# Kernel optimization log

Measured on AMD Instinct MI355X. Metric: run time of the kernel, lower is better.

## Reference

```python
import jax, jax.numpy as jnp
import numpy as np

LEAKY_ALPHA = 0.2  # LeakyReLU negative slope from init arg `alpha`


def setup_inputs() -> dict:
    key = jax.random.key(0)
    k1, k2, k3, k4 = jax.random.split(key, 4)
    B, N, Fin, Fout = 8, 2048, 256, 256
    h = jax.random.normal(k1, (B, N, Fin), dtype=jnp.float32)
    adj = jax.random.randint(k2, (N, N), 0, 2, dtype=jnp.int32)
    W = jax.random.normal(k3, (Fin, Fout), dtype=jnp.float32) * (1.414 * (6.0 / (Fin + Fout)) ** 0.5)
    a = jax.random.normal(k4, (2 * Fout, 1), dtype=jnp.float32) * (1.414 * (6.0 / (2 * Fout + 1)) ** 0.5)
    return {"h": h, "adj": adj, "W": W, "a": a}


def reference(h, adj, W, a):
    # h: (B, N, Fin), adj: (N, N) int {0,1}, W: (Fin, Fout), a: (2*Fout, 1)
    Fout = W.shape[1]
    Wh = jnp.einsum('bnf,fo->bno', h, W)            # (B, N, Fout)
    a1 = a[:Fout, 0]                                  # attends to target node i
    a2 = a[Fout:, 0]                                  # attends to source node j
    # a^T [Wh_i || Wh_j] == (Wh_i . a1) + (Wh_j . a2); LeakyReLU applied after, as in original
    s_i = Wh @ a1                                     # (B, N)
    s_j = Wh @ a2                                     # (B, N)
    e = jax.nn.leaky_relu(s_i[:, :, None] + s_j[:, None, :], negative_slope=LEAKY_ALPHA)  # (B, N, N)
    N = Wh.shape[1]
    mask = (adj > 0) | jnp.eye(N, dtype=bool)         # adjacency + self-loops
    e = jnp.where(mask[None, :, :], e, -jnp.inf)
    attention = jax.nn.softmax(e, axis=-1)            # dropout is identity in eval
    attention = jnp.nan_to_num(attention, nan=0.0)
    h_prime = jnp.einsum('bij,bjo->bio', attention, Wh)  # (B, N, Fout)
    return jax.nn.elu(h_prime)                        # concat=True -> ELU
```

## Files before the change

### kernel.cpp

```cpp
#include <hip/hip_runtime.h>

typedef unsigned short u16;
typedef unsigned int   u32;
typedef unsigned long long u64;

typedef __bf16 bf16x8 __attribute__((ext_vector_type(8)));
typedef float  f32x4  __attribute__((ext_vector_type(4)));

#define MFMA_BF16(a,b,c) __builtin_amdgcn_mfma_f32_16x16x32_bf16((a),(b),(c),0,0,0)

__device__ __forceinline__ float bf2f(u16 u) {
    return __uint_as_float(((u32)u) << 16);
}
__device__ __forceinline__ u16 f2bf(float x) {
    u32 u = __float_as_uint(x);
    u += 0x7fffu + ((u >> 16) & 1u);
    return (u16)(u >> 16);
}
__device__ __forceinline__ float ldany(const void* p, size_t i, int f32) {
    return f32 ? ((const float*)p)[i] : bf2f(((const u16*)p)[i]);
}
__device__ __forceinline__ int detect_f32(const u32* hw) {
    u32 w = hw[threadIdx.x & 63];
    int e = (w >> 23) & 0xFF;
    u64 m = __ballot(e >= 64 && e <= 190);
    return __popcll(m) >= 32 ? 1 : 0;
}

__global__ __launch_bounds__(256) void k0(const void* __restrict__ w, const void* __restrict__ a,
                                          u16* __restrict__ wt, float* __restrict__ wa1,
                                          float* __restrict__ wa2, const u32* __restrict__ hw) {
    int f32 = detect_f32(hw);
    int k = blockIdx.x, o = threadIdx.x;
    float wv = ldany(w, (size_t)k * 256 + o, f32);
    wt[o * 256 + k] = f2bf(wv);
    float p1 = wv * ldany(a, o, f32);
    float p2 = wv * ldany(a, 256 + o, f32);
    for (int d = 32; d; d >>= 1) { p1 += __shfl_down(p1, d); p2 += __shfl_down(p2, d); }
    __shared__ float s1[4], s2[4];
    int wid = o >> 6, lane = o & 63;
    if (lane == 0) { s1[wid] = p1; s2[wid] = p2; }
    __syncthreads();
    if (o == 0) { wa1[k] = s1[0] + s1[1] + s1[2] + s1[3]; wa2[k] = s2[0] + s2[1] + s2[2] + s2[3]; }
}

__global__ __launch_bounds__(256) void k1m(const int* __restrict__ adj, u64* __restrict__ mb64) {
    int t = threadIdx.x;
    int wv = t >> 6, lane = t & 63;
    #pragma unroll
    for (int q = 0; q < 4; q++) {
        int idx = blockIdx.x * 16 + wv * 4 + q;
        int mrow = idx >> 5, c = idx & 31;
        int j = c * 64 + lane;
        bool bit = (adj[(size_t)mrow * 2048 + j] > 0) || (j == mrow);
        u64 m = __ballot(bit);
        if (lane == 0) mb64[(size_t)mrow * 32 + c] = m;
    }
}

struct __align__(16) K2LDS {
    u16 At[64 * 68];
    union { u16 Bt[256 * 68]; u16 Ct[256 * 68]; };
    float wa1s[256], wa2s[256];
    float s1[64], s2[64];
};
__global__ __launch_bounds__(512) void k2(const void* __restrict__ h, const u16* __restrict__ wt,
                                          const float* __restrict__ wa1, const float* __restrict__ wa2,
                                          u16* __restrict__ whbt,
                                          float* __restrict__ sig, float* __restrict__ sjg) {
    __shared__ K2LDS L;
    int f32 = detect_f32((const u32*)h);
    int m0 = blockIdx.x * 64;
    int b  = m0 >> 11;
    int n0 = m0 & 2047;
    int t = threadIdx.x;
    int wid = t >> 6, lane = t & 63, ln = lane & 15, qd = lane >> 4;

    if (t < 256) { L.wa1s[t] = wa1[t]; L.wa2s[t] = wa2[t]; }
    if (t < 64) { L.s1[t] = 0.f; L.s2[t] = 0.f; }
    __syncthreads();

    float a1 = 0.f, a2 = 0.f;

    f32x4 acc[4][2];
    for (int mi = 0; mi < 4; mi++)
        for (int ni = 0; ni < 2; ni++)
            acc[mi][ni] = (f32x4){0.f, 0.f, 0.f, 0.f};

    for (int c = 0; c < 4; c++) {
        int k0c = c * 64;
        {
            int r = t >> 3, s = t & 7;
            float xv[8]; u16 uv[8];
            if (f32) {
                const float* src = (const float*)h + (size_t)(m0 + r) * 256 + k0c + s * 8;
                f32x4 x0 = *(const f32x4*)src;
                f32x4 x1 = *(const f32x4*)(src + 4);
                #pragma unroll
                for (int q = 0; q < 4; q++) { xv[q] = x0[q]; xv[4 + q] = x1[q]; }
                #pragma unroll
                for (int q = 0; q < 8; q++) uv[q] = f2bf(xv[q]);
            } else {
                const u16* src = (const u16*)h + (size_t)(m0 + r) * 256 + k0c + s * 8;
                *(uint4*)uv = *(const uint4*)src;
                #pragma unroll
                for (int q = 0; q < 8; q++) xv[q] = bf2f(uv[q]);
            }
            *(uint4*)&L.At[r * 68 + s * 8] = *(uint4*)uv;
            float pa = 0.f, pb = 0.f;
            #pragma unroll
            for (int q = 0; q < 8; q++) {
                pa += xv[q] * L.wa1s[k0c + s * 8 + q];
                pb += xv[q] * L.wa2s[k0c + s * 8 + q];
            }
            a1 += pa; a2 += pb;
        }
        #pragma unroll
        for (int p = 0; p < 4; p++) {
            int f = (t >> 3) + p * 64, s = t & 7;
            *(uint4*)&L.Bt[f * 68 + s * 8] =
                *(const uint4*)(wt + (size_t)f * 256 + k0c + s * 8);
        }
        __syncthreads();
        for (int ks = 0; ks < 2; ks++) {
            bf16x8 af[4], bfr[2];
            for (int mi = 0; mi < 4; mi++)
                af[mi] = *(const bf16x8*)&L.At[(mi * 16 + ln) * 68 + ks * 32 + qd * 8];
            for (int ni = 0; ni < 2; ni++)
                bfr[ni] = *(const bf16x8*)&L.Bt[(wid * 32 + ni * 16 + ln) * 68 + ks * 32 + qd * 8];
            for (int mi = 0; mi < 4; mi++)
                for (int ni = 0; ni < 2; ni++)
                    acc[mi][ni] = MFMA_BF16(af[mi], bfr[ni], acc[mi][ni]);
        }
        __syncthreads();
    }

    atomicAdd(&L.s1[t >> 3], a1);
    atomicAdd(&L.s2[t >> 3], a2);

    for (int mi = 0; mi < 4; mi++) {
        for (int ni = 0; ni < 2; ni++) {
            int f = wid * 32 + ni * 16 + ln;
            int n = mi * 16 + qd * 4;
            u16 v[4];
            for (int r = 0; r < 4; r++) v[r] = f2bf(acc[mi][ni][r]);
            *(uint2*)&L.Ct[f * 68 + n] = *(uint2*)v;
        }
    }
    __syncthreads();
    if (t < 64) { sig[m0 + t] = L.s1[t]; sjg[m0 + t] = L.s2[t]; }
    {
        int fr = t >> 1, hf = t & 1;
        size_t base = (size_t)b * 524288 + (size_t)fr * 2048 + n0;
        #pragma unroll
        for (int k = 0; k < 4; k++) {
            int s = hf * 4 + k;
            uint4 v = *(uint4*)&L.Ct[fr * 68 + s * 8];
            *(uint4*)(whbt + base + s * 8) = v;
        }
    }
}

__global__ __launch_bounds__(512) void k3n(const float* __restrict__ sig, const float* __restrict__ sjg,
                                           float* __restrict__ u1g, float* __restrict__ u2g,
                                           u32* __restrict__ vpackg, u16* __restrict__ sjbfg) {
    int b = blockIdx.x;
    int t = threadIdx.x;
    const float* sjb = sjg + (size_t)b * 2048;
    float mx = -3.4e38f;
    #pragma unroll
    for (int p = 0; p < 4; p++) mx = fmaxf(mx, sjb[t + p * 512]);
    for (int d = 32; d; d >>= 1) mx = fmaxf(mx, __shfl_xor(mx, d));
    __shared__ float wmax[8];
    int wid = t >> 6, lane = t & 63;
    if (lane == 0) wmax[wid] = mx;
    __syncthreads();
    float Mb = fmaxf(fmaxf(fmaxf(wmax[0], wmax[1]), fmaxf(wmax[2], wmax[3])),
                     fmaxf(fmaxf(wmax[4], wmax[5]), fmaxf(wmax[6], wmax[7])));
    #pragma unroll
    for (int p = 0; p < 4; p++) {
        int j = t + p * 512;
        float sjv = sjb[j];
        float vj  = __expf(sjv - Mb);
        float v2j = __expf(0.2f * (sjv - Mb));
        vpackg[b * 2048 + j] = (u32)f2bf(vj) | ((u32)f2bf(v2j) << 16);
        sjbfg[b * 2048 + j]  = f2bf(sjv);
        float siv = sig[b * 2048 + j];
        float x = siv + Mb;
        float K = fmaxf(x, 0.2f * x);
        u1g[b * 2048 + j] = __expf(x - K);
        u2g[b * 2048 + j] = __expf(0.2f * x - K);
    }
}

struct __align__(16) K4LDS {
    u32   vpack[2048];
    u16   sjb[2048];
    u64   mw[64 * 33];
    float u1[64], u2[64], nsi[64], inv[64];
    float lred[1024];
    u16   Pt[2][8192];
    int   claim[2];
};
__global__ __launch_bounds__(1024, 4) void k4(const float* __restrict__ sig,
                                              const float* __restrict__ u1g, const float* __restrict__ u2g,
                                              const u32* __restrict__ vpackg, const u16* __restrict__ sjbfg,
                                              const u64* __restrict__ mb64, const u16* __restrict__ whbt,
                                              void* __restrict__ out, const void* __restrict__ hdet,
                                              int* __restrict__ cnt) {
    __shared__ K4LDS L;
    int f32 = detect_f32((const u32*)hdet);
    int t = threadIdx.x;
    if (t == 0) {
        int xcd = __builtin_amdgcn_s_getreg(63508) & 7;
        int bsel = 0, tile = 0;
        #pragma unroll
        for (int k = 0; k < 8; k++) {
            int bb = (xcd + k) & 7;
            int tt = atomicAdd(&cnt[bb], 1);
            if (tt < 32) { bsel = bb; tile = tt; break; }
        }
        L.claim[0] = bsel; L.claim[1] = tile;
    }
    __syncthreads();
    int b  = L.claim[0];
    int i0 = L.claim[1] * 64;
    int wid = t >> 6, lane = t & 63, ln = lane & 15, qd = lane >> 4;
    const u16* wb = whbt + (size_t)b * 524288 + (size_t)wid * 16 * 2048;
    float lacc = 0.f;

    bf16x8 br[2][4];
    #define LOAD_B(cc, bb) do {                                             \
        int j0_ = (cc) * 128;                                               \
        _Pragma("unroll")                                                   \
        for (int ks = 0; ks < 4; ks++)                                      \
            br[bb][ks] = *(const bf16x8*)(wb +                              \
                (size_t)ln * 2048 + j0_ + ks * 32 + qd * 8);                \
    } while (0)

    #define PGEN(cc, bb) do {                                               \
        int r_ = t & 63, o_ = t >> 6;                                       \
        int jb_ = (cc) * 128 + o_ * 8;                                      \
        uint4 pkA_ = *(const uint4*)&L.vpack[jb_];                          \
        uint4 pkB_ = *(const uint4*)&L.vpack[jb_ + 4];                      \
        uint4 sj4_ = *(const uint4*)&L.sjb[jb_];                            \
        u32 mb_ = (u32)(L.mw[r_ * 33 + 2 * (cc) + (o_ >> 3)]                \
                        >> ((o_ & 7) * 8)) & 0xffu;                         \
        float u1_ = L.u1[r_], u2_ = L.u2[r_], nsi_ = L.nsi[r_];             \
        u32 pr_[4];                                                         \
        _Pragma("unroll")                                                   \
        for (int pk = 0; pk < 4; pk++) {                                    \
            u32 vw0_ = (pk == 0) ? pkA_.x : (pk == 1) ? pkA_.z              \
                     : (pk == 2) ? pkB_.x : pkB_.z;                         \
            u32 vw1_ = (pk == 0) ? pkA_.y : (pk == 1) ? pkA_.w              \
                     : (pk == 2) ? pkB_.y : pkB_.w;                         \
            u32 sw_ = (pk == 0) ? sj4_.x : (pk == 1) ? sj4_.y               \
                     : (pk == 2) ? sj4_.z : sj4_.w;                         \
            float sj0_ = __uint_as_float(sw_ << 16);                        \
            float sj1_ = __uint_as_float(sw_ & 0xffff0000u);                \
            float p0_, p1_;                                                 \
            {                                                               \
                bool pos = sj0_ > nsi_;                                     \
                float vv = __uint_as_float(pos ? (vw0_ << 16)               \
                                               : ((vw0_ >> 16) << 16));     \
                p0_ = (pos ? u1_ : u2_) * vv;                               \
                p0_ = ((mb_ >> (2 * pk)) & 1u) ? p0_ : 0.f;                 \
            }                                                               \
            {                                                               \
                bool pos = sj1_ > nsi_;                                     \
                float vv = __uint_as_float(pos ? (vw1_ << 16)               \
                                               : ((vw1_ >> 16) << 16));     \
                p1_ = (pos ? u1_ : u2_) * vv;                               \
                p1_ = ((mb_ >> (2 * pk + 1)) & 1u) ? p1_ : 0.f;             \
            }                                                               \
            lacc += p0_ + p1_;                                              \
            pr_[pk] = __builtin_amdgcn_perm(__float_as_uint(p1_),           \
                                            __float_as_uint(p0_),           \
                                            0x07060302u);                   \
        }                                                                   \
        *(uint4*)&L.Pt[bb][t * 8] = *(uint4*)pr_;                           \
    } while (0)

    LOAD_B(0, 0);
    for (int p = 0; p < 2; p++) { int idx = t + p * 1024; L.vpack[idx] = vpackg[b * 2048 + idx]; }
    ((u32*)L.sjb)[t] = ((const u32*)(sjbfg + (size_t)b * 2048))[t];
    for (int p = 0; p < 2; p++) {
        int idx = t + p * 1024;
        int r = idx >> 5, c = idx & 31;
        L.mw[r * 33 + c] = mb64[(size_t)(i0 + r) * 32 + c];
    }
    if (t < 64) {
        int row = b * 2048 + i0 + t;
        L.u1[t] = u1g[row]; L.u2[t] = u2g[row]; L.nsi[t] = -sig[row];
    }
    __syncthreads();
    PGEN(0, 0);

    f32x4 acc[4];
    for (int mi = 0; mi < 4; mi++)
        acc[mi] = (f32x4){0.f, 0.f, 0.f, 0.f};

    #define STEP(c, cur, nxt) do {                                          \
        __syncthreads();                                                    \
        if ((c) < 15) { LOAD_B((c) + 1, nxt); PGEN((c) + 1, nxt); }         \
        __builtin_amdgcn_s_setprio(1);                                      \
        _Pragma("unroll")                                                   \
        for (int ks = 0; ks < 4; ks++) {                                    \
            bf16x8 af[4];                                                   \
            _Pragma("unroll")                                               \
            for (int mi = 0; mi < 4; mi++)                                  \
                af[mi] = *(const bf16x8*)&L.Pt[cur][((ks * 4 + qd) * 64 +   \
                                                     mi * 16 + ln) * 8];    \
            _Pragma("unroll")                                               \
            for (int mi = 0; mi < 4; mi++)                                  \
                acc[mi] = MFMA_BF16(af[mi], br[cur][ks], acc[mi]);          \
        }                                                                   \
        __builtin_amdgcn_s_setprio(0);                                      \
    } while (0)

    for (int cc = 0; cc < 8; cc++) {
        STEP(2 * cc,     0, 1);
        STEP(2 * cc + 1, 1, 0);
    }

    __syncthreads();
    L.lred[t] = lacc;
    __syncthreads();
    if (t < 64) {
        float s = 0.f;
        #pragma unroll
        for (int q = 0; q < 16; q++) s += L.lred[q * 64 + t];
        L.inv[t] = 1.0f / s;
    }
    __syncthreads();

    {
        int fg = wid * 16 + ln;
        for (int mi = 0; mi < 4; mi++) {
            for (int reg = 0; reg < 4; reg++) {
                int rl = mi * 16 + qd * 4 + reg;
                float hp = acc[mi][reg] * L.inv[rl];
                float y = hp > 0.f ? hp : (__expf(hp) - 1.f);
                size_t idx = (size_t)(b * 2048 + i0 + rl) * 256 + fg;
                if (f32) ((float*)out)[idx] = y;
                else     ((u16*)out)[idx]   = f2bf(y);
            }
        }
    }
    #undef LOAD_B
    #undef PGEN
    #undef STEP
}

extern "C" void kernel_launch(void* const* d_in, const int* in_sizes, int n_in,
                              void* d_out, int out_size, void* d_ws, size_t ws_size,
                              hipStream_t stream) {
    const void* h   = d_in[0];
    const int*  adj = (const int*)d_in[1];
    const void* W   = d_in[2];
    const void* a   = d_in[3];

    char* ws = (char*)d_ws;
    u16*   WT    = (u16*)  (ws + 0);
    float* si    = (float*)(ws + 131072);
    float* sj    = (float*)(ws + 196608);
    float* u1    = (float*)(ws + 262144);
    float* u2    = (float*)(ws + 327680);
    u32*   vpack = (u32*)  (ws + 458752);
    u16*   sjbf  = (u16*)  (ws + 524288);
    u64*   mb64  = (u64*)  (ws + 557056);
    u16*   whbt  = (u16*)  (ws + 1081344);
    float* Wa1   = (float*)(ws + 9469952);
    float* Wa2   = (float*)(ws + 9470976);
    int*   cnt   = (int*)  (ws + 9472000);

    hipMemsetAsync(cnt, 0, 32, stream);
    k0 <<<dim3(256),  dim3(256), 0, stream>>>(W, a, WT, Wa1, Wa2, (const u32*)h);
    k1m<<<dim3(4096), dim3(256), 0, stream>>>(adj, mb64);
    k2 <<<dim3(256),  dim3(512), 0, stream>>>(h, WT, Wa1, Wa2, whbt, si, sj);
    k3n<<<dim3(8),    dim3(512), 0, stream>>>(si, sj, u1, u2, vpack, sjbf);
    k4 <<<dim3(256),  dim3(1024), 0, stream>>>(si, u1, u2, vpack, sjbf, mb64, whbt, d_out, h, cnt);
}
```

Baseline: 139.2 us.

## Fuse all stages into one cooperative persistent kernel with grid syncs

Replaces the memset and five separate kernel launches with a single cooperative kernel of 256 blocks x 1024 threads. Stages are separated by grid-wide syncs and share one LDS union. The mask-packing stage is restructured so each wave batches 16 loads before its ballots, and the projection GEMM now splits threads into an h-loading group and a W-loading group. This removes launch gaps and the memset, at the cost of grid-sync overhead and running the small stages at fixed 1024-thread occupancy.

New measurement: 237.6 us. +70.7%, slower.

```diff
diff --git a/kernel.cpp b/kernel.cpp
--- a/kernel.cpp
+++ b/kernel.cpp
@@ -1,4 +1,7 @@
 #include <hip/hip_runtime.h>
+#include <hip/hip_cooperative_groups.h>
+
+namespace cg = cooperative_groups;
 
 typedef unsigned short u16;
 typedef unsigned int   u32;
@@ -25,37 +28,6 @@
     int e = (w >> 23) & 0xFF;
     u64 m = __ballot(e >= 64 && e <= 190);
     return __popcll(m) >= 32 ? 1 : 0;
-}
-
-__global__ __launch_bounds__(256) void k0(const void* __restrict__ w, const void* __restrict__ a,
-                                          u16* __restrict__ wt, float* __restrict__ wa1,
-                                          float* __restrict__ wa2, const u32* __restrict__ hw) {
-    int f32 = detect_f32(hw);
-    int k = blockIdx.x, o = threadIdx.x;
-    float wv = ldany(w, (size_t)k * 256 + o, f32);
-    wt[o * 256 + k] = f2bf(wv);
-    float p1 = wv * ldany(a, o, f32);
-    float p2 = wv * ldany(a, 256 + o, f32);
-    for (int d = 32; d; d >>= 1) { p1 += __shfl_down(p1, d); p2 += __shfl_down(p2, d); }
-    __shared__ float s1[4], s2[4];
-    int wid = o >> 6, lane = o & 63;
-    if (lane == 0) { s1[wid] = p1; s2[wid] = p2; }
-    __syncthreads();
-    if (o == 0) { wa1[k] = s1[0] + s1[1] + s1[2] + s1[3]; wa2[k] = s2[0] + s2[1] + s2[2] + s2[3]; }
-}
-
-__global__ __launch_bounds__(256) void k1m(const int* __restrict__ adj, u64* __restrict__ mb64) {
-    int t = threadIdx.x;
-    int wv = t >> 6, lane = t & 63;
-    #pragma unroll
-    for (int q = 0; q < 4; q++) {
-        int idx = blockIdx.x * 16 + wv * 4 + q;
-        int mrow = idx >> 5, c = idx & 31;
-        int j = c * 64 + lane;
-        bool bit = (adj[(size_t)mrow * 2048 + j] > 0) || (j == mrow);
-        u64 m = __ballot(bit);
-        if (lane == 0) mb64[(size_t)mrow * 32 + c] = m;
-    }
 }
 
 struct __align__(16) K2LDS {
@@ -64,135 +36,6 @@
     float wa1s[256], wa2s[256];
     float s1[64], s2[64];
 };
-__global__ __launch_bounds__(512) void k2(const void* __restrict__ h, const u16* __restrict__ wt,
-                                          const float* __restrict__ wa1, const float* __restrict__ wa2,
-                                          u16* __restrict__ whbt,
-                                          float* __restrict__ sig, float* __restrict__ sjg) {
-    __shared__ K2LDS L;
-    int f32 = detect_f32((const u32*)h);
-    int m0 = blockIdx.x * 64;
-    int b  = m0 >> 11;
-    int n0 = m0 & 2047;
-    int t = threadIdx.x;
-    int wid = t >> 6, lane = t & 63, ln = lane & 15, qd = lane >> 4;
-
-    if (t < 256) { L.wa1s[t] = wa1[t]; L.wa2s[t] = wa2[t]; }
-    if (t < 64) { L.s1[t] = 0.f; L.s2[t] = 0.f; }
-    __syncthreads();
-
-    float a1 = 0.f, a2 = 0.f;
-
-    f32x4 acc[4][2];
-    for (int mi = 0; mi < 4; mi++)
-        for (int ni = 0; ni < 2; ni++)
-            acc[mi][ni] = (f32x4){0.f, 0.f, 0.f, 0.f};
-
-    for (int c = 0; c < 4; c++) {
-        int k0c = c * 64;
-        {
-            int r = t >> 3, s = t & 7;
-            float xv[8]; u16 uv[8];
-            if (f32) {
-                const float* src = (const float*)h + (size_t)(m0 + r) * 256 + k0c + s * 8;
-                f32x4 x0 = *(const f32x4*)src;
-                f32x4 x1 = *(const f32x4*)(src + 4);
-                #pragma unroll
-                for (int q = 0; q < 4; q++) { xv[q] = x0[q]; xv[4 + q] = x1[q]; }
-                #pragma unroll
-                for (int q = 0; q < 8; q++) uv[q] = f2bf(xv[q]);
-            } else {
-                const u16* src = (const u16*)h + (size_t)(m0 + r) * 256 + k0c + s * 8;
-                *(uint4*)uv = *(const uint4*)src;
-                #pragma unroll
-                for (int q = 0; q < 8; q++) xv[q] = bf2f(uv[q]);
-            }
-            *(uint4*)&L.At[r * 68 + s * 8] = *(uint4*)uv;
-            float pa = 0.f, pb = 0.f;
-            #pragma unroll
-            for (int q = 0; q < 8; q++) {
-                pa += xv[q] * L.wa1s[k0c + s * 8 + q];
-                pb += xv[q] * L.wa2s[k0c + s * 8 + q];
-            }
-            a1 += pa; a2 += pb;
-        }
-        #pragma unroll
-        for (int p = 0; p < 4; p++) {
-            int f = (t >> 3) + p * 64, s = t & 7;
-            *(uint4*)&L.Bt[f * 68 + s * 8] =
-                *(const uint4*)(wt + (size_t)f * 256 + k0c + s * 8);
-        }
-        __syncthreads();
-        for (int ks = 0; ks < 2; ks++) {
-            bf16x8 af[4], bfr[2];
-            for (int mi = 0; mi < 4; mi++)
-                af[mi] = *(const bf16x8*)&L.At[(mi * 16 + ln) * 68 + ks * 32 + qd * 8];
-            for (int ni = 0; ni < 2; ni++)
-                bfr[ni] = *(const bf16x8*)&L.Bt[(wid * 32 + ni * 16 + ln) * 68 + ks * 32 + qd * 8];
-            for (int mi = 0; mi < 4; mi++)
-                for (int ni = 0; ni < 2; ni++)
-                    acc[mi][ni] = MFMA_BF16(af[mi], bfr[ni], acc[mi][ni]);
-        }
-        __syncthreads();
-    }
-
-    atomicAdd(&L.s1[t >> 3], a1);
-    atomicAdd(&L.s2[t >> 3], a2);
-
-    for (int mi = 0; mi < 4; mi++) {
-        for (int ni = 0; ni < 2; ni++) {
-            int f = wid * 32 + ni * 16 + ln;
-            int n = mi * 16 + qd * 4;
-            u16 v[4];
-            for (int r = 0; r < 4; r++) v[r] = f2bf(acc[mi][ni][r]);
-            *(uint2*)&L.Ct[f * 68 + n] = *(uint2*)v;
-        }
-    }
-    __syncthreads();
-    if (t < 64) { sig[m0 + t] = L.s1[t]; sjg[m0 + t] = L.s2[t]; }
-    {
-        int fr = t >> 1, hf = t & 1;
-        size_t base = (size_t)b * 524288 + (size_t)fr * 2048 + n0;
-        #pragma unroll
-        for (int k = 0; k < 4; k++) {
-            int s = hf * 4 + k;
-            uint4 v = *(uint4*)&L.Ct[fr * 68 + s * 8];
-            *(uint4*)(whbt + base + s * 8) = v;
-        }
-    }
-}
-
-__global__ __launch_bounds__(512) void k3n(const float* __restrict__ sig, const float* __restrict__ sjg,
-                                           float* __restrict__ u1g, float* __restrict__ u2g,
-                                           u32* __restrict__ vpackg, u16* __restrict__ sjbfg) {
-    int b = blockIdx.x;
-    int t = threadIdx.x;
-    const float* sjb = sjg + (size_t)b * 2048;
-    float mx = -3.4e38f;
-    #pragma unroll
-    for (int p = 0; p < 4; p++) mx = fmaxf(mx, sjb[t + p * 512]);
-    for (int d = 32; d; d >>= 1) mx = fmaxf(mx, __shfl_xor(mx, d));
-    __shared__ float wmax[8];
-    int wid = t >> 6, lane = t & 63;
-    if (lane == 0) wmax[wid] = mx;
-    __syncthreads();
-    float Mb = fmaxf(fmaxf(fmaxf(wmax[0], wmax[1]), fmaxf(wmax[2], wmax[3])),
-                     fmaxf(fmaxf(wmax[4], wmax[5]), fmaxf(wmax[6], wmax[7])));
-    #pragma unroll
-    for (int p = 0; p < 4; p++) {
-        int j = t + p * 512;
-        float sjv = sjb[j];
-        float vj  = __expf(sjv - Mb);
-        float v2j = __expf(0.2f * (sjv - Mb));
-        vpackg[b * 2048 + j] = (u32)f2bf(vj) | ((u32)f2bf(v2j) << 16);
-        sjbfg[b * 2048 + j]  = f2bf(sjv);
-        float siv = sig[b * 2048 + j];
-        float x = siv + Mb;
-        float K = fmaxf(x, 0.2f * x);
-        u1g[b * 2048 + j] = __expf(x - K);
-        u2g[b * 2048 + j] = __expf(0.2f * x - K);
-    }
-}
-
 struct __align__(16) K4LDS {
     u32   vpack[2048];
     u16   sjb[2048];
@@ -202,154 +45,328 @@
     u16   Pt[2][8192];
     int   claim[2];
 };
-__global__ __launch_bounds__(1024, 4) void k4(const float* __restrict__ sig,
-                                              const float* __restrict__ u1g, const float* __restrict__ u2g,
-                                              const u32* __restrict__ vpackg, const u16* __restrict__ sjbfg,
-                                              const u64* __restrict__ mb64, const u16* __restrict__ whbt,
-                                              void* __restrict__ out, const void* __restrict__ hdet,
-                                              int* __restrict__ cnt) {
-    __shared__ K4LDS L;
-    int f32 = detect_f32((const u32*)hdet);
-    int t = threadIdx.x;
-    if (t == 0) {
-        int xcd = __builtin_amdgcn_s_getreg(63508) & 7;
-        int bsel = 0, tile = 0;
+struct __align__(16) FusedLDS {
+    union {
+        struct { float s1[16], s2[16]; } p0;
+        struct { float wmax[16]; } p3;
+        K2LDS p2;
+        K4LDS p4;
+    };
+};
+
+__global__ __launch_bounds__(1024, 4) void fused(
+        const void* __restrict__ h, const int* __restrict__ adj,
+        const void* __restrict__ w, const void* __restrict__ a,
+        u16* __restrict__ wt, float* __restrict__ wa1, float* __restrict__ wa2,
+        float* __restrict__ sig, float* __restrict__ sjg,
+        float* __restrict__ u1g, float* __restrict__ u2g,
+        u32* __restrict__ vpackg, u16* __restrict__ sjbfg,
+        u64* __restrict__ mb64, u16* __restrict__ whbt,
+        void* __restrict__ out, int* __restrict__ cnt) {
+    __shared__ FusedLDS U;
+    cg::grid_group gg = cg::this_grid();
+    int f32 = detect_f32((const u32*)h);
+    int t = threadIdx.x, bid = blockIdx.x;
+    int wid = t >> 6, lane = t & 63, ln = lane & 15, qd = lane >> 4;
+
+    if (bid < 64) {
+        int g = t >> 8, o = t & 255;
+        int k = bid * 4 + g;
+        float wv = ldany(w, (size_t)k * 256 + o, f32);
+        wt[o * 256 + k] = f2bf(wv);
+        float p1 = wv * ldany(a, o, f32);
+        float p2 = wv * ldany(a, 256 + o, f32);
+        for (int d = 32; d; d >>= 1) { p1 += __shfl_down(p1, d); p2 += __shfl_down(p2, d); }
+        if (lane == 0) { U.p0.s1[wid] = p1; U.p0.s2[wid] = p2; }
+        __syncthreads();
+        if (o == 0) {
+            wa1[k] = U.p0.s1[g * 4] + U.p0.s1[g * 4 + 1] + U.p0.s1[g * 4 + 2] + U.p0.s1[g * 4 + 3];
+            wa2[k] = U.p0.s2[g * 4] + U.p0.s2[g * 4 + 1] + U.p0.s2[g * 4 + 2] + U.p0.s2[g * 4 + 3];
+        }
+    }
+    if (bid == 0 && t < 8) cnt[t] = 0;
+
+    {
+        int base = bid * 256 + wid * 16;
+        u32 va[16];
         #pragma unroll
-        for (int k = 0; k < 8; k++) {
-            int bb = (xcd + k) & 7;
-            int tt = atomicAdd(&cnt[bb], 1);
-            if (tt < 32) { bsel = bb; tile = tt; break; }
-        }
-        L.claim[0] = bsel; L.claim[1] = tile;
+        for (int q = 0; q < 16; q++) {
+            int idx = base + q;
+            int mrow = idx >> 5, c = idx & 31;
+            int j = c * 64 + lane;
+            va[q] = (u32)(adj[(size_t)mrow * 2048 + j] > 0) | (u32)(j == mrow);
+        }
+        #pragma unroll
+        for (int q = 0; q < 16; q++) {
+            u64 m = __ballot(va[q] != 0);
+            if (lane == 0) mb64[base + q] = m;
+        }
     }
-    __syncthreads();
-    int b  = L.claim[0];
-    int i0 = L.claim[1] * 64;
-    int wid = t >> 6, lane = t & 63, ln = lane & 15, qd = lane >> 4;
-    const u16* wb = whbt + (size_t)b * 524288 + (size_t)wid * 16 * 2048;
-    float lacc = 0.f;
-
-    bf16x8 br[2][4];
-    #define LOAD_B(cc, bb) do {                                             \
-        int j0_ = (cc) * 128;                                               \
-        _Pragma("unroll")                                                   \
-        for (int ks = 0; ks < 4; ks++)                                      \
-            br[bb][ks] = *(const bf16x8*)(wb +                              \
-                (size_t)ln * 2048 + j0_ + ks * 32 + qd * 8);                \
-    } while (0)
-
-    #define PGEN(cc, bb) do {                                               \
-        int r_ = t & 63, o_ = t >> 6;                                       \
-        int jb_ = (cc) * 128 + o_ * 8;                                      \
-        uint4 pkA_ = *(const uint4*)&L.vpack[jb_];                          \
-        uint4 pkB_ = *(const uint4*)&L.vpack[jb_ + 4];                      \
-        uint4 sj4_ = *(const uint4*)&L.sjb[jb_];                            \
-        u32 mb_ = (u32)(L.mw[r_ * 33 + 2 * (cc) + (o_ >> 3)]                \
-                        >> ((o_ & 7) * 8)) & 0xffu;                         \
-        float u1_ = L.u1[r_], u2_ = L.u2[r_], nsi_ = L.nsi[r_];             \
-        u32 pr_[4];                                                         \
-        _Pragma("unroll")                                                   \
-        for (int pk = 0; pk < 4; pk++) {                                    \
-            u32 vw0_ = (pk == 0) ? pkA_.x : (pk == 1) ? pkA_.z              \
-                     : (pk == 2) ? pkB_.x : pkB_.z;                         \
-            u32 vw1_ = (pk == 0) ? pkA_.y : (pk == 1) ? pkA_.w              \
-                     : (pk == 2) ? pkB_.y : pkB_.w;                         \
-            u32 sw_ = (pk == 0) ? sj4_.x : (pk == 1) ? sj4_.y               \
-                     : (pk == 2) ? sj4_.z : sj4_.w;                         \
-            float sj0_ = __uint_as_float(sw_ << 16);                        \
-            float sj1_ = __uint_as_float(sw_ & 0xffff0000u);                \
-            float p0_, p1_;                                                 \
-            {                                                               \
-                bool pos = sj0_ > nsi_;                                     \
-                float vv = __uint_as_float(pos ? (vw0_ << 16)               \
-                                               : ((vw0_ >> 16) << 16));     \
-                p0_ = (pos ? u1_ : u2_) * vv;                               \
-                p0_ = ((mb_ >> (2 * pk)) & 1u) ? p0_ : 0.f;                 \
-            }                                                               \
-            {                                                               \
-                bool pos = sj1_ > nsi_;                                     \
-                float vv = __uint_as_float(pos ? (vw1_ << 16)               \
-                                               : ((vw1_ >> 16) << 16));     \
-                p1_ = (pos ? u1_ : u2_) * vv;                               \
-                p1_ = ((mb_ >> (2 * pk + 1)) & 1u) ? p1_ : 0.f;             \
-            }                                                               \
-            lacc += p0_ + p1_;                                              \
-            pr_[pk] = __builtin_amdgcn_perm(__float_as_uint(p1_),           \
-                                            __float_as_uint(p0_),           \
-                                            0x07060302u);                   \
-        }                                                                   \
-        *(uint4*)&L.Pt[bb][t * 8] = *(uint4*)pr_;                           \
-    } while (0)
-
-    LOAD_B(0, 0);
-    for (int p = 0; p < 2; p++) { int idx = t + p * 1024; L.vpack[idx] = vpackg[b * 2048 + idx]; }
-    ((u32*)L.sjb)[t] = ((const u32*)(sjbfg + (size_t)b * 2048))[t];
-    for (int p = 0; p < 2; p++) {
-        int idx = t + p * 1024;
-        int r = idx >> 5, c = idx & 31;
-        L.mw[r * 33 + c] = mb64[(size_t)(i0 + r) * 32 + c];
+
+    gg.sync();
+
+    {
+        K2LDS& L = U.p2;
+        int m0 = bid * 64;
+        int b  = m0 >> 11;
+        int n0 = m0 & 2047;
+        if (t < 256) { L.wa1s[t] = wa1[t]; L.wa2s[t] = wa2[t]; }
+        if (t < 64) { L.s1[t] = 0.f; L.s2[t] = 0.f; }
+        __syncthreads();
+
+        float a1 = 0.f, a2 = 0.f;
+        f32x4 acc[4];
+        for (int mi = 0; mi < 4; mi++) acc[mi] = (f32x4){0.f, 0.f, 0.f, 0.f};
+
+        for (int c = 0; c < 4; c++) {
+            int k0c = c * 64;
+            if (t < 512) {
+                int r = t >> 3, s = t & 7;
+                float xv[8]; u16 uv[8];
+                if (f32) {
+                    const float* src = (const float*)h + (size_t)(m0 + r) * 256 + k0c + s * 8;
+                    f32x4 x0 = *(const f32x4*)src;
+                    f32x4 x1 = *(const f32x4*)(src + 4);
+                    #pragma unroll
+                    for (int q = 0; q < 4; q++) { xv[q] = x0[q]; xv[4 + q] = x1[q]; }
+                    #pragma unroll
+                    for (int q = 0; q < 8; q++) uv[q] = f2bf(xv[q]);
+                } else {
+                    const u16* src = (const u16*)h + (size_t)(m0 + r) * 256 + k0c + s * 8;
+                    *(uint4*)uv = *(const uint4*)src;
+                    #pragma unroll
+                    for (int q = 0; q < 8; q++) xv[q] = bf2f(uv[q]);
+                }
+                *(uint4*)&L.At[r * 68 + s * 8] = *(uint4*)uv;
+                float pa = 0.f, pb = 0.f;
+                #pragma unroll
+                for (int q = 0; q < 8; q++) {
+                    pa += xv[q] * L.wa1s[k0c + s * 8 + q];
+                    pb += xv[q] * L.wa2s[k0c + s * 8 + q];
+                }
+                a1 += pa; a2 += pb;
+            } else {
+                int tt = t - 512;
+                #pragma unroll
+                for (int p = 0; p < 4; p++) {
+                    int f = (tt >> 3) + p * 64, s = tt & 7;
+                    *(uint4*)&L.Bt[f * 68 + s * 8] =
+                        *(const uint4*)(wt + (size_t)f * 256 + k0c + s * 8);
+                }
+            }
+            __syncthreads();
+            for (int ks = 0; ks < 2; ks++) {
+                bf16x8 af[4], bfr;
+                for (int mi = 0; mi < 4; mi++)
+                    af[mi] = *(const bf16x8*)&L.At[(mi * 16 + ln) * 68 + ks * 32 + qd * 8];
+                bfr = *(const bf16x8*)&L.Bt[(wid * 16 + ln) * 68 + ks * 32 + qd * 8];
+                for (int mi = 0; mi < 4; mi++)
+                    acc[mi] = MFMA_BF16(af[mi], bfr, acc[mi]);
+            }
+            __syncthreads();
+        }
+
+        if (t < 512) {
+            atomicAdd(&L.s1[t >> 3], a1);
+            atomicAdd(&L.s2[t >> 3], a2);
+        }
+        for (int mi = 0; mi < 4; mi++) {
+            int f = wid * 16 + ln;
+            int n = mi * 16 + qd * 4;
+            u16 v[4];
+            for (int r = 0; r < 4; r++) v[r] = f2bf(acc[mi][r]);
+            *(uint2*)&L.Ct[f * 68 + n] = *(uint2*)v;
+        }
+        __syncthreads();
+        if (t < 64) { sig[m0 + t] = L.s1[t]; sjg[m0 + t] = L.s2[t]; }
+        {
+            int fr = t >> 2, q0 = (t & 3) * 2;
+            size_t base = (size_t)b * 524288 + (size_t)fr * 2048 + n0;
+            #pragma unroll
+            for (int k = 0; k < 2; k++) {
+                int s = q0 + k;
+                uint4 v = *(uint4*)&L.Ct[fr * 68 + s * 8];
+                *(uint4*)(whbt + base + s * 8) = v;
+            }
+        }
     }
-    if (t < 64) {
-        int row = b * 2048 + i0 + t;
-        L.u1[t] = u1g[row]; L.u2[t] = u2g[row]; L.nsi[t] = -sig[row];
+
+    gg.sync();
+
+    if (bid < 8) {
+        const float* sjb = sjg + (size_t)bid * 2048;
+        float mx = -3.4e38f;
+        if (t < 512) {
+            #pragma unroll
+            for (int p = 0; p < 4; p++) mx = fmaxf(mx, sjb[t + p * 512]);
+        }
+        for (int d = 32; d; d >>= 1) mx = fmaxf(mx, __shfl_xor(mx, d));
+        if (lane == 0) U.p3.wmax[wid] = mx;
+        __syncthreads();
+        float Mb = -3.4e38f;
+        #pragma unroll
+        for (int q = 0; q < 16; q++) Mb = fmaxf(Mb, U.p3.wmax[q]);
+        if (t < 512) {
+            #pragma unroll
+            for (int p = 0; p < 4; p++) {
+                int j = t + p * 512;
+                float sjv = sjb[j];
+                float vj  = __expf(sjv - Mb);
+                float v2j = __expf(0.2f * (sjv - Mb));
+                vpackg[bid * 2048 + j] = (u32)f2bf(vj) | ((u32)f2bf(v2j) << 16);
+                sjbfg[bid * 2048 + j]  = f2bf(sjv);
+                float siv = sig[bid * 2048 + j];
+                float x = siv + Mb;
+                float K = fmaxf(x, 0.2f * x);
+                u1g[bid * 2048 + j] = __expf(x - K);
+                u2g[bid * 2048 + j] = __expf(0.2f * x - K);
+            }
+        }
     }
-    __syncthreads();
-    PGEN(0, 0);
-
-    f32x4 acc[4];
-    for (int mi = 0; mi < 4; mi++)
-        acc[mi] = (f32x4){0.f, 0.f, 0.f, 0.f};
-
-    #define STEP(c, cur, nxt) do {                                          \
-        __syncthreads();                                                    \
-        if ((c) < 15) { LOAD_B((c) + 1, nxt); PGEN((c) + 1, nxt); }         \
-        __builtin_amdgcn_s_setprio(1);                                      \
-        _Pragma("unroll")                                                   \
-        for (int ks = 0; ks < 4; ks++) {                                    \
-            bf16x8 af[4];                                                   \
-            _Pragma("unroll")                                               \
-            for (int mi = 0; mi < 4; mi++)                                  \
-                af[mi] = *(const bf16x8*)&L.Pt[cur][((ks * 4 + qd) * 64 +   \
-                                                     mi * 16 + ln) * 8];    \
-            _Pragma("unroll")                                               \
-            for (int mi = 0; mi < 4; mi++)                                  \
-                acc[mi] = MFMA_BF16(af[mi], br[cur][ks], acc[mi]);          \
-        }                                                                   \
-        __builtin_amdgcn_s_setprio(0);                                      \
-    } while (0)
-
-    for (int cc = 0; cc < 8; cc++) {
-        STEP(2 * cc,     0, 1);
-        STEP(2 * cc + 1, 1, 0);
+
+    gg.sync();
+
+    {
+        K4LDS& L = U.p4;
+        if (t == 0) {
+            int xcd = __builtin_amdgcn_s_getreg(63508) & 7;
+            int bsel = 0, tile = 0;
+            #pragma unroll
+            for (int k = 0; k < 8; k++) {
+                int bb = (xcd + k) & 7;
+                int tt = atomicAdd(&cnt[bb], 1);
+                if (tt < 32) { bsel = bb; tile = tt; break; }
+            }
+            L.claim[0] = bsel; L.claim[1] = tile;
+        }
+        __syncthreads();
+        int b  = L.claim[0];
+        int i0 = L.claim[1] * 64;
+        const u16* wb = whbt + (size_t)b * 524288 + (size_t)wid * 16 * 2048;
+        float lacc = 0.f;
+
+        bf16x8 br[2][4];
+        #define LOAD_B(cc, bb) do {                                             \
+            int j0_ = (cc) * 128;                                               \
+            _Pragma("unroll")                                                   \
+            for (int ks = 0; ks < 4; ks++)                                      \
+                br[bb][ks] = *(const bf16x8*)(wb +                              \
+                    (size_t)ln * 2048 + j0_ + ks * 32 + qd * 8);                \
+        } while (0)
+
+        #define PGEN(cc, bb) do {                                               \
+            int r_ = t & 63, o_ = t >> 6;                                       \
+            int jb_ = (cc) * 128 + o_ * 8;                                      \
+            uint4 pkA_ = *(const uint4*)&L.vpack[jb_];                          \
+            uint4 pkB_ = *(const uint4*)&L.vpack[jb_ + 4];                      \
+            uint4 sj4_ = *(const uint4*)&L.sjb[jb_];                            \
+            u32 mb_ = (u32)(L.mw[r_ * 33 + 2 * (cc) + (o_ >> 3)]                \
+                            >> ((o_ & 7) * 8)) & 0xffu;                         \
+            float u1_ = L.u1[r_], u2_ = L.u2[r_], nsi_ = L.nsi[r_];             \
+            u32 pr_[4];                                                         \
+            _Pragma("unroll")                                                   \
+            for (int pk = 0; pk < 4; pk++) {                                    \
+                u32 vw0_ = (pk == 0) ? pkA_.x : (pk == 1) ? pkA_.z              \
+                         : (pk == 2) ? pkB_.x : pkB_.z;                         \
+                u32 vw1_ = (pk == 0) ? pkA_.y : (pk == 1) ? pkA_.w              \
+                         : (pk == 2) ? pkB_.y : pkB_.w;                         \
+                u32 sw_ = (pk == 0) ? sj4_.x : (pk == 1) ? sj4_.y               \
+                         : (pk == 2) ? sj4_.z : sj4_.w;                         \
+                float sj0_ = __uint_as_float(sw_ << 16);                        \
+                float sj1_ = __uint_as_float(sw_ & 0xffff0000u);                \
+                float p0_, p1_;                                                 \
+                {                                                               \
+                    bool pos = sj0_ > nsi_;                                     \
+                    float vv = __uint_as_float(pos ? (vw0_ << 16)               \
+                                                   : ((vw0_ >> 16) << 16));     \
+                    p0_ = (pos ? u1_ : u2_) * vv;                               \
+                    p0_ = ((mb_ >> (2 * pk)) & 1u) ? p0_ : 0.f;                 \
+                }                                                               \
+                {                                                               \
+                    bool pos = sj1_ > nsi_;                                     \
+                    float vv = __uint_as_float(pos ? (vw1_ << 16)               \
+                                                   : ((vw1_ >> 16) << 16));     \
+                    p1_ = (pos ? u1_ : u2_) * vv;                               \
+                    p1_ = ((mb_ >> (2 * pk + 1)) & 1u) ? p1_ : 0.f;             \
+                }                                                               \
+                lacc += p0_ + p1_;                                              \
+                pr_[pk] = __builtin_amdgcn_perm(__float_as_uint(p1_),           \
+                                                __float_as_uint(p0_),           \
+                                                0x07060302u);                   \
+            }                                                                   \
+            *(uint4*)&L.Pt[bb][t * 8] = *(uint4*)pr_;                           \
+        } while (0)
+
+        LOAD_B(0, 0);
+        for (int p = 0; p < 2; p++) { int idx = t + p * 1024; L.vpack[idx] = vpackg[b * 2048 + idx]; }
+        ((u32*)L.sjb)[t] = ((const u32*)(sjbfg + (size_t)b * 2048))[t];
+        for (int p = 0; p < 2; p++) {
+            int idx = t + p * 1024;
+            int r = idx >> 5, c = idx & 31;
+            L.mw[r * 33 + c] = mb64[(size_t)(i0 + r) * 32 + c];
+        }
+        if (t < 64) {
+            int row = b * 2048 + i0 + t;
+            L.u1[t] = u1g[row]; L.u2[t] = u2g[row]; L.nsi[t] = -sig[row];
+        }
+        __syncthreads();
+        PGEN(0, 0);
+
+        f32x4 acc[4];
+        for (int mi = 0; mi < 4; mi++)
+            acc[mi] = (f32x4){0.f, 0.f, 0.f, 0.f};
+
+        #define STEP(c, cur, nxt) do {                                          \
+            __syncthreads();                                                    \
+            if ((c) < 15) { LOAD_B((c) + 1, nxt); PGEN((c) + 1, nxt); }         \
+            __builtin_amdgcn_s_setprio(1);                                      \
+            _Pragma("unroll")                                                   \
+            for (int ks = 0; ks < 4; ks++) {                                    \
+                bf16x8 af[4];                                                   \
+                _Pragma("unroll")                                               \
+                for (int mi = 0; mi < 4; mi++)                                  \
+                    af[mi] = *(const bf16x8*)&L.Pt[cur][((ks * 4 + qd) * 64 +   \
+                                                         mi * 16 + ln) * 8];    \
+                _Pragma("unroll")                                               \
+                for (int mi = 0; mi < 4; mi++)                                  \
+                    acc[mi] = MFMA_BF16(af[mi], br[cur][ks], acc[mi]);          \
+            }                                                                   \
+            __builtin_amdgcn_s_setprio(0);                                      \
+        } while (0)
+
+        for (int cc = 0; cc < 8; cc++) {
+            STEP(2 * cc,     0, 1);
+            STEP(2 * cc + 1, 1, 0);
+        }
+
+        __syncthreads();
+        L.lred[t] = lacc;
+        __syncthreads();
+        if (t < 64) {
+            float s = 0.f;
+            #pragma unroll
+            for (int q = 0; q < 16; q++) s += L.lred[q * 64 + t];
+            L.inv[t] = 1.0f / s;
+        }
+        __syncthreads();
+
+        {
+            int fg = wid * 16 + ln;
+            for (int mi = 0; mi < 4; mi++) {
+                for (int reg = 0; reg < 4; reg++) {
+                    int rl = mi * 16 + qd * 4 + reg;
+                    float hp = acc[mi][reg] * L.inv[rl];
+                    float y = hp > 0.f ? hp : (__expf(hp) - 1.f);
+                    size_t idx = (size_t)(b * 2048 + i0 + rl) * 256 + fg;
+                    if (f32) ((float*)out)[idx] = y;
+                    else     ((u16*)out)[idx]   = f2bf(y);
+                }
+            }
+        }
+        #undef LOAD_B
+        #undef PGEN
+        #undef STEP
     }
-
-    __syncthreads();
-    L.lred[t] = lacc;
-    __syncthreads();
-    if (t < 64) {
-        float s = 0.f;
-        #pragma unroll
-        for (int q = 0; q < 16; q++) s += L.lred[q * 64 + t];
-        L.inv[t] = 1.0f / s;
-    }
-    __syncthreads();
-
-    {
-        int fg = wid * 16 + ln;
-        for (int mi = 0; mi < 4; mi++) {
-            for (int reg = 0; reg < 4; reg++) {
-                int rl = mi * 16 + qd * 4 + reg;
-                float hp = acc[mi][reg] * L.inv[rl];
-                float y = hp > 0.f ? hp : (__expf(hp) - 1.f);
-                size_t idx = (size_t)(b * 2048 + i0 + rl) * 256 + fg;
-                if (f32) ((float*)out)[idx] = y;
-                else     ((u16*)out)[idx]   = f2bf(y);
-            }
-        }
-    }
-    #undef LOAD_B
-    #undef PGEN
-    #undef STEP
 }
 
 extern "C" void kernel_launch(void* const* d_in, const int* in_sizes, int n_in,
@@ -374,10 +391,13 @@
     float* Wa2   = (float*)(ws + 9470976);
     int*   cnt   = (int*)  (ws + 9472000);
 
-    hipMemsetAsync(cnt, 0, 32, stream);
-    k0 <<<dim3(256),  dim3(256), 0, stream>>>(W, a, WT, Wa1, Wa2, (const u32*)h);
-    k1m<<<dim3(4096), dim3(256), 0, stream>>>(adj, mb64);
-    k2 <<<dim3(256),  dim3(512), 0, stream>>>(h, WT, Wa1, Wa2, whbt, si, sj);
-    k3n<<<dim3(8),    dim3(512), 0, stream>>>(si, sj, u1, u2, vpack, sjbf);
-    k4 <<<dim3(256),  dim3(1024), 0, stream>>>(si, u1, u2, vpack, sjbf, mb64, whbt, d_out, h, cnt);
-}
+    void* outp = d_out;
+    void* kargs[] = {
+        (void*)&h, (void*)&adj, (void*)&W, (void*)&a,
+        (void*)&WT, (void*)&Wa1, (void*)&Wa2, (void*)&si, (void*)&sj,
+        (void*)&u1, (void*)&u2, (void*)&vpack, (void*)&sjbf,
+        (void*)&mb64, (void*)&whbt, (void*)&outp, (void*)&cnt
+    };
+    hipLaunchCooperativeKernel((const void*)fused, dim3(256), dim3(1024),
+                               kargs, 0, stream);
+}
```

## Merge prep kernels and fold per-batch softmax normalization into attention kernel

Applied to the files above, without the earlier changes.

Combines the weight-transpose/projection kernel, the adjacency bitmask kernel and the counter memset into a single launch, and removes the separate per-batch max/exp kernel by recomputing the max of s_j and the exponent tables inside each attention block. This cuts three launches plus the intermediate global buffers. The cost is that each of the 256 attention blocks redoes a 2048-element reduction and 4096 exponentials, and adds an extra block barrier before PGEN.

After: 132.8 us. 4.6% less time.

```diff
diff --git a/kernel.cpp b/kernel.cpp
--- a/kernel.cpp
+++ b/kernel.cpp
@@ -27,34 +27,37 @@
     return __popcll(m) >= 32 ? 1 : 0;
 }
 
-__global__ __launch_bounds__(256) void k0(const void* __restrict__ w, const void* __restrict__ a,
-                                          u16* __restrict__ wt, float* __restrict__ wa1,
-                                          float* __restrict__ wa2, const u32* __restrict__ hw) {
-    int f32 = detect_f32(hw);
-    int k = blockIdx.x, o = threadIdx.x;
-    float wv = ldany(w, (size_t)k * 256 + o, f32);
-    wt[o * 256 + k] = f2bf(wv);
-    float p1 = wv * ldany(a, o, f32);
-    float p2 = wv * ldany(a, 256 + o, f32);
-    for (int d = 32; d; d >>= 1) { p1 += __shfl_down(p1, d); p2 += __shfl_down(p2, d); }
+__global__ __launch_bounds__(256) void kprep(const void* __restrict__ w, const void* __restrict__ a,
+                                             const int* __restrict__ adj,
+                                             u16* __restrict__ wt, float* __restrict__ wa1,
+                                             float* __restrict__ wa2, u64* __restrict__ mb64,
+                                             int* __restrict__ cnt, const u32* __restrict__ hw) {
     __shared__ float s1[4], s2[4];
-    int wid = o >> 6, lane = o & 63;
-    if (lane == 0) { s1[wid] = p1; s2[wid] = p2; }
-    __syncthreads();
-    if (o == 0) { wa1[k] = s1[0] + s1[1] + s1[2] + s1[3]; wa2[k] = s2[0] + s2[1] + s2[2] + s2[3]; }
-}
-
-__global__ __launch_bounds__(256) void k1m(const int* __restrict__ adj, u64* __restrict__ mb64) {
-    int t = threadIdx.x;
-    int wv = t >> 6, lane = t & 63;
-    #pragma unroll
-    for (int q = 0; q < 4; q++) {
-        int idx = blockIdx.x * 16 + wv * 4 + q;
-        int mrow = idx >> 5, c = idx & 31;
-        int j = c * 64 + lane;
-        bool bit = (adj[(size_t)mrow * 2048 + j] > 0) || (j == mrow);
-        u64 m = __ballot(bit);
-        if (lane == 0) mb64[(size_t)mrow * 32 + c] = m;
+    int bid = blockIdx.x, t = threadIdx.x;
+    int wid = t >> 6, lane = t & 63;
+    if (bid < 256) {
+        if (bid == 0 && t < 8) cnt[t] = 0;
+        int f32 = detect_f32(hw);
+        int k = bid, o = t;
+        float wv = ldany(w, (size_t)k * 256 + o, f32);
+        wt[o * 256 + k] = f2bf(wv);
+        float p1 = wv * ldany(a, o, f32);
+        float p2 = wv * ldany(a, 256 + o, f32);
+        for (int d = 32; d; d >>= 1) { p1 += __shfl_down(p1, d); p2 += __shfl_down(p2, d); }
+        if (lane == 0) { s1[wid] = p1; s2[wid] = p2; }
+        __syncthreads();
+        if (o == 0) { wa1[k] = s1[0] + s1[1] + s1[2] + s1[3]; wa2[k] = s2[0] + s2[1] + s2[2] + s2[3]; }
+    } else {
+        int b2 = bid - 256;
+        #pragma unroll
+        for (int q = 0; q < 4; q++) {
+            int idx = b2 * 16 + wid * 4 + q;
+            int mrow = idx >> 5, c = idx & 31;
+            int j = c * 64 + lane;
+            bool bit = (adj[(size_t)mrow * 2048 + j] > 0) || (j == mrow);
+            u64 m = __ballot(bit);
+            if (lane == 0) mb64[(size_t)mrow * 32 + c] = m;
+        }
     }
 }
 
@@ -161,38 +164,6 @@
     }
 }
 
-__global__ __launch_bounds__(512) void k3n(const float* __restrict__ sig, const float* __restrict__ sjg,
-                                           float* __restrict__ u1g, float* __restrict__ u2g,
-                                           u32* __restrict__ vpackg, u16* __restrict__ sjbfg) {
-    int b = blockIdx.x;
-    int t = threadIdx.x;
-    const float* sjb = sjg + (size_t)b * 2048;
-    float mx = -3.4e38f;
-    #pragma unroll
-    for (int p = 0; p < 4; p++) mx = fmaxf(mx, sjb[t + p * 512]);
-    for (int d = 32; d; d >>= 1) mx = fmaxf(mx, __shfl_xor(mx, d));
-    __shared__ float wmax[8];
-    int wid = t >> 6, lane = t & 63;
-    if (lane == 0) wmax[wid] = mx;
-    __syncthreads();
-    float Mb = fmaxf(fmaxf(fmaxf(wmax[0], wmax[1]), fmaxf(wmax[2], wmax[3])),
-                     fmaxf(fmaxf(wmax[4], wmax[5]), fmaxf(wmax[6], wmax[7])));
-    #pragma unroll
-    for (int p = 0; p < 4; p++) {
-        int j = t + p * 512;
-        float sjv = sjb[j];
-        float vj  = __expf(sjv - Mb);
-        float v2j = __expf(0.2f * (sjv - Mb));
-        vpackg[b * 2048 + j] = (u32)f2bf(vj) | ((u32)f2bf(v2j) << 16);
-        sjbfg[b * 2048 + j]  = f2bf(sjv);
-        float siv = sig[b * 2048 + j];
-        float x = siv + Mb;
-        float K = fmaxf(x, 0.2f * x);
-        u1g[b * 2048 + j] = __expf(x - K);
-        u2g[b * 2048 + j] = __expf(0.2f * x - K);
-    }
-}
-
 struct __align__(16) K4LDS {
     u32   vpack[2048];
     u16   sjb[2048];
@@ -203,8 +174,7 @@
     int   claim[2];
 };
 __global__ __launch_bounds__(1024, 4) void k4(const float* __restrict__ sig,
-                                              const float* __restrict__ u1g, const float* __restrict__ u2g,
-                                              const u32* __restrict__ vpackg, const u16* __restrict__ sjbfg,
+                                              const float* __restrict__ sjg,
                                               const u64* __restrict__ mb64, const u16* __restrict__ whbt,
                                               void* __restrict__ out, const void* __restrict__ hdet,
                                               int* __restrict__ cnt) {
@@ -282,16 +252,42 @@
     } while (0)
 
     LOAD_B(0, 0);
-    for (int p = 0; p < 2; p++) { int idx = t + p * 1024; L.vpack[idx] = vpackg[b * 2048 + idx]; }
-    ((u32*)L.sjb)[t] = ((const u32*)(sjbfg + (size_t)b * 2048))[t];
+    float sjv0 = sjg[b * 2048 + t];
+    float sjv1 = sjg[b * 2048 + 1024 + t];
+    {
+        float mx = fmaxf(sjv0, sjv1);
+        for (int d = 32; d; d >>= 1) mx = fmaxf(mx, __shfl_xor(mx, d));
+        if (lane == 0) L.lred[wid] = mx;
+    }
     for (int p = 0; p < 2; p++) {
         int idx = t + p * 1024;
         int r = idx >> 5, c = idx & 31;
         L.mw[r * 33 + c] = mb64[(size_t)(i0 + r) * 32 + c];
     }
+    __syncthreads();
+    float Mb;
+    {
+        float m0_ = fmaxf(fmaxf(fmaxf(L.lred[0], L.lred[1]), fmaxf(L.lred[2], L.lred[3])),
+                          fmaxf(fmaxf(L.lred[4], L.lred[5]), fmaxf(L.lred[6], L.lred[7])));
+        float m1_ = fmaxf(fmaxf(fmaxf(L.lred[8], L.lred[9]), fmaxf(L.lred[10], L.lred[11])),
+                          fmaxf(fmaxf(L.lred[12], L.lred[13]), fmaxf(L.lred[14], L.lred[15])));
+        Mb = fmaxf(m0_, m1_);
+    }
+    {
+        float vj0 = __expf(sjv0 - Mb), v2j0 = __expf(0.2f * (sjv0 - Mb));
+        L.vpack[t] = (u32)f2bf(vj0) | ((u32)f2bf(v2j0) << 16);
+        L.sjb[t] = f2bf(sjv0);
+        float vj1 = __expf(sjv1 - Mb), v2j1 = __expf(0.2f * (sjv1 - Mb));
+        L.vpack[t + 1024] = (u32)f2bf(vj1) | ((u32)f2bf(v2j1) << 16);
+        L.sjb[t + 1024] = f2bf(sjv1);
+    }
     if (t < 64) {
-        int row = b * 2048 + i0 + t;
-        L.u1[t] = u1g[row]; L.u2[t] = u2g[row]; L.nsi[t] = -sig[row];
+        float siv = sig[b * 2048 + i0 + t];
+        float x = siv + Mb;
+        float K = fmaxf(x, 0.2f * x);
+        L.u1[t] = __expf(x - K);
+        L.u2[t] = __expf(0.2f * x - K);
+        L.nsi[t] = -siv;
     }
     __syncthreads();
     PGEN(0, 0);
@@ -364,20 +360,13 @@
     u16*   WT    = (u16*)  (ws + 0);
     float* si    = (float*)(ws + 131072);
     float* sj    = (float*)(ws + 196608);
-    float* u1    = (float*)(ws + 262144);
-    float* u2    = (float*)(ws + 327680);
-    u32*   vpack = (u32*)  (ws + 458752);
-    u16*   sjbf  = (u16*)  (ws + 524288);
     u64*   mb64  = (u64*)  (ws + 557056);
     u16*   whbt  = (u16*)  (ws + 1081344);
     float* Wa1   = (float*)(ws + 9469952);
     float* Wa2   = (float*)(ws + 9470976);
     int*   cnt   = (int*)  (ws + 9472000);
 
-    hipMemsetAsync(cnt, 0, 32, stream);
-    k0 <<<dim3(256),  dim3(256), 0, stream>>>(W, a, WT, Wa1, Wa2, (const u32*)h);
-    k1m<<<dim3(4096), dim3(256), 0, stream>>>(adj, mb64);
-    k2 <<<dim3(256),  dim3(512), 0, stream>>>(h, WT, Wa1, Wa2, whbt, si, sj);
-    k3n<<<dim3(8),    dim3(512), 0, stream>>>(si, sj, u1, u2, vpack, sjbf);
-    k4 <<<dim3(256),  dim3(1024), 0, stream>>>(si, u1, u2, vpack, sjbf, mb64, whbt, d_out, h, cnt);
-}
+    kprep<<<dim3(4352), dim3(256),  0, stream>>>(W, a, adj, WT, Wa1, Wa2, mb64, cnt, (const u32*)h);
+    k2   <<<dim3(256),  dim3(512),  0, stream>>>(h, WT, Wa1, Wa2, whbt, si, sj);
+    k4   <<<dim3(256),  dim3(1024), 0, stream>>>(si, sj, mb64, whbt, d_out, h, cnt);
+}
```
